# Kernel optimization log

Measured on AMD Instinct MI355X. Metric: run time of the kernel, lower is better.

The kernel has to match this reference:

```python
import jax, jax.numpy as jnp
import numpy as np

NUM_HEADS = 8

def rotate_half(x):
    # interleaved rotate: pairs (x0,x1)->(-x1,x0)
    x1 = x[..., ::2]
    x2 = x[..., 1::2]
    return jnp.stack((-x2, x1), axis=-1).reshape(x.shape)

def rope_cos_sin(seq_len, head_dim, dtype, base=10000.0):
    idx = jnp.arange(0, head_dim, 2, dtype=dtype)
    inv_freq = 1.0 / base ** (idx / head_dim)
    t = jnp.arange(seq_len, dtype=dtype)
    freqs = t[:, None] * inv_freq[None, :]            # (L, hd/2)
    emb = jnp.concatenate([freqs, freqs], axis=-1)    # (L, hd) -- NOTE: cat, not interleave (faithful to source)
    return jnp.cos(emb)[None, None], jnp.sin(emb)[None, None]  # (1,1,L,hd)

def setup_inputs() -> dict:
    key = jax.random.key(0)
    ks = jax.random.split(key, 5)
    B, L, C = 2, 4096, 512
    s_in = 1.0 / np.sqrt(C)
    return {
        "x": jax.random.normal(ks[0], (B, L, C), dtype=jnp.float32),
        "qkv_w": jax.random.normal(ks[1], (3 * C, C), dtype=jnp.float32) * s_in,
        "qkv_b": jnp.zeros((3 * C,), dtype=jnp.float32),
        "proj_w": jax.random.normal(ks[2], (C, C), dtype=jnp.float32) * s_in,
        "proj_b": jnp.zeros((C,), dtype=jnp.float32),
    }

def reference(x, qkv_w, qkv_b, proj_w, proj_b):
    B, L, C = x.shape
    H = NUM_HEADS
    hd = C // H
    scale = hd ** -0.5
    qkv = x @ qkv_w.T + qkv_b                          # (B,L,3C)
    qkv = qkv.reshape(B, L, 3, H, hd).transpose(2, 0, 3, 1, 4)  # (3,B,H,L,hd)
    q, k, v = qkv[0], qkv[1], qkv[2]
    cos, sin = rope_cos_sin(L, hd, x.dtype)
    q = q * cos + rotate_half(q) * sin
    k = k * cos + rotate_half(k) * sin
    attn = jnp.einsum('bhqd,bhkd->bhqk', q, k) * scale  # (B,H,L,L)
    attn = jax.nn.softmax(attn, axis=-1)
    out = jnp.einsum('bhqk,bhkd->bhqd', attn, v)        # (B,H,L,hd)
    out = out.transpose(0, 2, 1, 3).reshape(B, L, C)
    return out @ proj_w.T + proj_b
```

## Files before the change

### kernel.cpp

```cpp
#include <hip/hip_runtime.h>
#include <hip/hip_bf16.h>


typedef __attribute__((ext_vector_type(8))) short short8;
typedef __attribute__((ext_vector_type(4))) short short4v;
typedef __attribute__((ext_vector_type(4))) float floatx4;

#define MFMA(a, b, c)   __builtin_amdgcn_mfma_f32_16x16x32_bf16((a), (b), (c), 0, 0, 0)
#define MFMA16(a, b, c) __builtin_amdgcn_mfma_f32_16x16x16bf16_1k((a), (b), (c), 0, 0, 0)

__device__ __forceinline__ float fast_exp2(float x) {
#if __has_builtin(__builtin_amdgcn_exp2f)
    return __builtin_amdgcn_exp2f(x);
#else
    float r; asm("v_exp_f32 %0, %1" : "=v"(r) : "v"(x)); return r;
#endif
}

__device__ __forceinline__ unsigned short f2bf(float f) {
    unsigned int u = __builtin_bit_cast(unsigned int, f);
    return (unsigned short)((u + 0x7fffu + ((u >> 16) & 1u)) >> 16);
}
__device__ __forceinline__ unsigned int pack2(float lo, float hi) {
    __hip_bfloat162 h = __float22bfloat162_rn(make_float2(lo, hi));
    unsigned int r;
    __builtin_memcpy(&r, &h, 4);
    return r;
}

__global__ __launch_bounds__(256) void conv_pack(
    const float* __restrict__ src, ushort* __restrict__ dst, int n8)
{
    int i = blockIdx.x * blockDim.x + threadIdx.x;
    if (i >= n8) return;
    const int row = i >> 6, col0 = (i & 63) * 8;
    const float4* s = (const float4*)(src + (size_t)row * 512 + col0);
    float4 a = s[0], b = s[1];
    uint4 r = { pack2(a.x, a.y), pack2(a.z, a.w), pack2(b.x, b.y), pack2(b.z, b.w) };
    const int l = (row & 15) + 16 * ((col0 >> 3) & 3);
    const size_t off = (size_t)(row >> 4) * 8192 + (size_t)(col0 >> 5) * 512 + l * 8;
    *(uint4*)(dst + off) = r;
}

__global__ __launch_bounds__(256) void build_rope(float2* __restrict__ lut) {
    int i = blockIdx.x * 256 + threadIdx.x;
    int pos = i >> 5, j = i & 31;
    float invf = exp2f(-0.41524101186f * (float)j);
    float s, c;
    sincosf((float)pos * invf, &s, &c);
    lut[i] = make_float2(c, s);
}

__global__ __launch_bounds__(256) void qkv_rope(
    const ushort* __restrict__ xb,
    const ushort* __restrict__ wb,
    const float* __restrict__ bias,
    const float2* __restrict__ lut,
    ushort* __restrict__ q, ushort* __restrict__ k, ushort* __restrict__ vt,
    int G, int h0)
{
    __shared__ __align__(16) ushort vtile[64][136];
    const int w_id = threadIdx.x >> 6;
    const int lane = threadIdx.x & 63;
    const int lr = lane & 15, quad = lane >> 4;
    const int m0 = blockIdx.x * 128 + w_id * 32;
    const int sec = blockIdx.y / G, hl = blockIdx.y % G;
    const int wc0 = sec * 512 + (h0 + hl) * 64;

    floatx4 acc[2][4] = {};
    const ushort* xa = xb + (size_t)(m0 >> 4) * 8192 + lane * 8;
    const ushort* wbase = wb + (size_t)(wc0 >> 4) * 8192 + lane * 8;
    for (int kk = 0; kk < 16; ++kk) {
        short8 a0 = *(const short8*)(xa + kk * 512);
        short8 a1 = *(const short8*)(xa + 8192 + kk * 512);
#pragma unroll
        for (int nt = 0; nt < 4; ++nt) {
            short8 b = *(const short8*)(wbase + (size_t)nt * 8192 + kk * 512);
            acc[0][nt] = MFMA(a0, b, acc[0][nt]);
            acc[1][nt] = MFMA(a1, b, acc[1][nt]);
        }
    }

    if (sec < 2) {
#pragma unroll
        for (int mt = 0; mt < 2; ++mt)
#pragma unroll
            for (int nt = 0; nt < 4; ++nt) {
                const int d = nt * 16 + lr;
                const float bv = bias[wc0 + d];
#pragma unroll
                for (int r = 0; r < 4; ++r) {
                    const int row = m0 + mt * 16 + quad * 4 + r;
                    const int b_ = row >> 12;
                    const int pos = row & 4095;
                    float val = acc[mt][nt][r] + bv;
                    const size_t bhl = (size_t)(b_ * G + hl);
                    float partner = __shfl_xor(val, 1);
                    float2 cs = lut[(pos << 5) | (d & 31)];
                    float rh = (d & 1) ? partner : -partner;
                    float rv = val * cs.x + rh * cs.y;
                    if (sec == 0) {
                        rv *= 0.18033688011112042f;
                        q[(bhl * 4096 + pos) * 64 + d] = f2bf(rv);
                    } else {
                        const int idx = (pos >> 5) * 2048 + ((pos >> 4) & 1) * 1024
                                      + (d >> 5) * 512 + ((d >> 3) & 3) * 128
                                      + (pos & 15) * 8 + (d & 7);
                        k[bhl * 262144 + idx] = f2bf(rv);
                    }
                }
            }
    } else {
#pragma unroll
        for (int mt = 0; mt < 2; ++mt)
#pragma unroll
            for (int nt = 0; nt < 4; ++nt) {
                const int d = nt * 16 + lr;
                const float bv = bias[wc0 + d];
                short4v v4;
#pragma unroll
                for (int r = 0; r < 4; ++r)
                    v4[r] = (short)f2bf(acc[mt][nt][r] + bv);
                *(short4v*)&vtile[d][w_id * 32 + mt * 16 + quad * 4] = v4;
            }
        __syncthreads();
        const int m0b = blockIdx.x * 128;
        const int bb = m0b >> 12;
        const int pos0 = m0b & 4095;
        const size_t bhl = (size_t)(bb * G + hl);
        const int dt = w_id;
        ushort* vb = vt + bhl * 262144 + dt * 512 + lane * 8;
#pragma unroll
        for (int j = 0; j < 4; ++j) {
            const int col = j * 32 + quad * 4;
            short4v a = *(const short4v*)&vtile[dt * 16 + lr][col];
            short4v b = *(const short4v*)&vtile[dt * 16 + lr][col + 16];
            short8 vv = __builtin_shufflevector(a, b, 0, 1, 2, 3, 4, 5, 6, 7);
            *(short8*)(vb + ((pos0 >> 5) + j) * 2048) = vv;
        }
    }
}

__global__ __launch_bounds__(256, 3) void flash_attn(
    const ushort* __restrict__ q, const ushort* __restrict__ k,
    const ushort* __restrict__ vt, ushort* __restrict__ o,
    int G, int h0)
{
    __shared__ __align__(16) float mb[65][33];
    const int kh = threadIdx.x >> 6;
    const int lane = threadIdx.x & 63;
    const int lr = lane & 15, quad = lane >> 4;
    const int nbh = 2 * G;
    const int bhl = blockIdx.x % nbh;
    const int qtile = blockIdx.x / nbh;
    const int b_ = bhl / G, hl = bhl % G;
    const int q0 = qtile * 32;

    const ushort* qp = q + (size_t)bhl * 262144;
    const int hcol = (h0 + hl) * 64;
    ushort* opp = o + (size_t)(((b_ << 12) + q0) >> 4) * 8192 + (hcol >> 5) * 512;
    const ushort* kpw = k + (size_t)bhl * 262144 + kh * 65536 + lane * 8;
    const ushort* vpw = vt + (size_t)bhl * 262144 + kh * 65536 + lane * 8;

    short8 qf[2][2];
#pragma unroll
    for (int nn = 0; nn < 2; ++nn) {
        const ushort* qb = qp + (size_t)(q0 + 16 * nn + lr) * 64 + quad * 8;
        qf[nn][0] = *(const short8*)qb;
        qf[nn][1] = *(const short8*)(qb + 32);
    }

    floatx4 oacc[4][2] = {};
    float lsum[2] = {0.f, 0.f};
    short8 ka0[2][2], ka1[2][2];
    short8 va[4];

    auto ldK = [&](int c, short8 (&ka)[2][2]) {
        const ushort* kb = kpw + c * 2048;
        ka[0][0] = *(const short8*)(kb);
        ka[0][1] = *(const short8*)(kb + 512);
        ka[1][0] = *(const short8*)(kb + 1024);
        ka[1][1] = *(const short8*)(kb + 1536);
    };
    auto ldV = [&](int c) {
        const ushort* vb = vpw + c * 2048;
#pragma unroll
        for (int dt = 0; dt < 4; ++dt)
            va[dt] = *(const short8*)(vb + dt * 512);
    };
    auto process = [&](short8 (&ka)[2][2]) {
#pragma unroll
        for (int t = 0; t < 2; ++t) {
#pragma unroll
            for (int nn = 0; nn < 2; ++nn) {
                floatx4 s = {};
                s = MFMA(ka[t][0], qf[nn][0], s);
                s = MFMA(ka[t][1], qf[nn][1], s);
                float p0 = fast_exp2(s[0]), p1 = fast_exp2(s[1]);
                float p2 = fast_exp2(s[2]), p3 = fast_exp2(s[3]);
                lsum[nn] += (p0 + p1) + (p2 + p3);
                uint2 u = { pack2(p0, p1), pack2(p2, p3) };
                short4v pf = __builtin_bit_cast(short4v, u);
#pragma unroll
                for (int dt = 0; dt < 4; ++dt) {
                    short4v vf = (t == 0)
                        ? __builtin_shufflevector(va[dt], va[dt], 0, 1, 2, 3)
                        : __builtin_shufflevector(va[dt], va[dt], 4, 5, 6, 7);
                    oacc[dt][nn] = MFMA16(vf, pf, oacc[dt][nn]);
                }
            }
        }
    };

    ldK(0, ka0);
    for (int it = 0; it < 30; it += 2) {
        ldV(it);
        ldK(it + 1, ka1);
        process(ka0);
        ldV(it + 1);
        ldK(it + 2, ka0);
        process(ka1);
    }
    ldV(30); ldK(31, ka1); process(ka0);
    ldV(31); process(ka1);

    lsum[0] += __shfl_xor(lsum[0], 16); lsum[0] += __shfl_xor(lsum[0], 32);
    lsum[1] += __shfl_xor(lsum[1], 16); lsum[1] += __shfl_xor(lsum[1], 32);

    __syncthreads();
    if (kh == 3) {
#pragma unroll
        for (int dt = 0; dt < 4; ++dt)
#pragma unroll
            for (int nn = 0; nn < 2; ++nn)
#pragma unroll
                for (int r = 0; r < 4; ++r)
                    mb[16 * dt + 4 * quad + r][16 * nn + lr] = oacc[dt][nn][r];
        if (quad == 0) {
            mb[64][lr] = lsum[0];
            mb[64][16 + lr] = lsum[1];
        }
    }
    __syncthreads();
    if (kh == 2) {
#pragma unroll
        for (int dt = 0; dt < 4; ++dt)
#pragma unroll
            for (int nn = 0; nn < 2; ++nn)
#pragma unroll
                for (int r = 0; r < 4; ++r)
                    mb[16 * dt + 4 * quad + r][16 * nn + lr] += oacc[dt][nn][r];
        if (quad == 0) {
            mb[64][lr] += lsum[0];
            mb[64][16 + lr] += lsum[1];
        }
    }
    __syncthreads();
    if (kh == 1) {
#pragma unroll
        for (int dt = 0; dt < 4; ++dt)
#pragma unroll
            for (int nn = 0; nn < 2; ++nn)
#pragma unroll
                for (int r = 0; r < 4; ++r)
                    mb[16 * dt + 4 * quad + r][16 * nn + lr] += oacc[dt][nn][r];
        if (quad == 0) {
            mb[64][lr] += lsum[0];
            mb[64][16 + lr] += lsum[1];
        }
    }
    __syncthreads();
    if (kh == 0) {
        float inv0 = 1.0f / (lsum[0] + mb[64][lr]);
        float inv1 = 1.0f / (lsum[1] + mb[64][16 + lr]);
#pragma unroll
        for (int dt = 0; dt < 4; ++dt)
#pragma unroll
            for (int nn = 0; nn < 2; ++nn) {
                float inv = nn ? inv1 : inv0;
                float v0 = (oacc[dt][nn][0] + mb[16 * dt + 4 * quad + 0][16 * nn + lr]) * inv;
                float v1 = (oacc[dt][nn][1] + mb[16 * dt + 4 * quad + 1][16 * nn + lr]) * inv;
                float v2 = (oacc[dt][nn][2] + mb[16 * dt + 4 * quad + 2][16 * nn + lr]) * inv;
                float v3 = (oacc[dt][nn][3] + mb[16 * dt + 4 * quad + 3][16 * nn + lr]) * inv;
                uint2 u = { pack2(v0, v1), pack2(v2, v3) };
                const int cg = 16 * dt + 4 * quad;
                *(uint2*)(opp + (size_t)nn * 8192 + (cg >> 5) * 512
                          + (lr + 16 * ((cg >> 3) & 3)) * 8 + (cg & 7)) = u;
            }
    }
}

__global__ __launch_bounds__(256) void proj_gemm(
    const ushort* __restrict__ o,
    const ushort* __restrict__ wb,
    const float* __restrict__ bias,
    float* __restrict__ out)
{
    const int w_id = threadIdx.x >> 6;
    const int lane = threadIdx.x & 63;
    const int lr = lane & 15, quad = lane >> 4;
    const int m0 = blockIdx.x * 128 + w_id * 32;
    const int n0 = blockIdx.y * 64;

    floatx4 acc[2][4] = {};
    const ushort* oa = o + (size_t)(m0 >> 4) * 8192 + lane * 8;
    const ushort* wbase = wb + (size_t)(n0 >> 4) * 8192 + lane * 8;
    for (int kk = 0; kk < 16; ++kk) {
        short8 a0 = *(const short8*)(oa + kk * 512);
        short8 a1 = *(const short8*)(oa + 8192 + kk * 512);
#pragma unroll
        for (int nt = 0; nt < 4; ++nt) {
            short8 b = *(const short8*)(wbase + (size_t)nt * 8192 + kk * 512);
            acc[0][nt] = MFMA(a0, b, acc[0][nt]);
            acc[1][nt] = MFMA(a1, b, acc[1][nt]);
        }
    }
#pragma unroll
    for (int mt = 0; mt < 2; ++mt)
#pragma unroll
        for (int nt = 0; nt < 4; ++nt) {
            const int n = n0 + nt * 16 + lr;
            const float bv = bias[n];
#pragma unroll
            for (int r = 0; r < 4; ++r)
                out[(size_t)(m0 + mt * 16 + quad * 4 + r) * 512 + n] = acc[mt][nt][r] + bv;
        }
}

extern "C" void kernel_launch(void* const* d_in, const int* in_sizes, int n_in,
                              void* d_out, int out_size, void* d_ws, size_t ws_size,
                              hipStream_t stream)
{
    const float* x      = (const float*)d_in[0];
    const float* qkv_w  = (const float*)d_in[1];
    const float* qkv_b  = (const float*)d_in[2];
    const float* proj_w = (const float*)d_in[3];
    const float* proj_b = (const float*)d_in[4];
    float* out = (float*)d_out;

    const size_t MB = (size_t)1 << 20;
    ushort* base = (ushort*)d_ws;
    int G;
    ushort *xb, *o, *wb, *pwb, *q, *k, *vt;
    if (ws_size >= 34 * MB) {
        G = 8;
        xb = base; o = base;
        wb  = base + 4194304;
        pwb = wb + 786432;
        q   = pwb + 262144;
        k   = q + (size_t)G * 524288;
        vt  = k + (size_t)G * 524288;
    } else {
        G = (ws_size >= 30 * MB) ? 4 : (ws_size >= 24 * MB) ? 2 : 1;
        xb  = base;
        o   = base + 4194304;
        wb  = o + 4194304;
        pwb = wb + 786432;
        q   = pwb + 262144;
        k   = q + (size_t)G * 524288;
        vt  = k + (size_t)G * 524288;
    }

    float2* lut = (float2*)d_out;
    build_rope<<<512, 256, 0, stream>>>(lut);

    conv_pack<<<2048, 256, 0, stream>>>(x, xb, 524288);
    conv_pack<<<384, 256, 0, stream>>>(qkv_w, wb, 98304);
    conv_pack<<<128, 256, 0, stream>>>(proj_w, pwb, 32768);

    for (int h0 = 0; h0 < 8; h0 += G) {
        qkv_rope<<<dim3(64, 3 * G), 256, 0, stream>>>(xb, wb, qkv_b, lut, q, k, vt, G, h0);
        flash_attn<<<128 * 2 * G, 256, 0, stream>>>(q, k, vt, o, G, h0);
    }
    proj_gemm<<<dim3(64, 8), 256, 0, stream>>>(o, pwb, proj_b, out);
}
```

Measured before the change: 219.9 us.

## Switch flash attention to 32x32x16 MFMA with matching K/V layouts

Replaces the 16x16 MFMA tiling in the attention kernel with 32x32x16 bf16 MFMAs. A single 32x32 score tile now covers all 32 queries, and the PV product accumulates into two 16-float accumulators. The K and V^T global layouts written by the QKV kernel are re-swizzled so each lane's 8-element loads feed the 32x32 operand layout directly, and the epilogue reduction and output store are remapped to match. This is meant to cut MFMA issue count and per-instruction overhead, at the cost of larger accumulators and a different register and exp scheduling pattern.

```diff
diff --git a/kernel.cpp b/kernel.cpp
--- a/kernel.cpp
+++ b/kernel.cpp
@@ -2,12 +2,13 @@
 #include <hip/hip_bf16.h>
 
 
-typedef __attribute__((ext_vector_type(8))) short short8;
-typedef __attribute__((ext_vector_type(4))) short short4v;
-typedef __attribute__((ext_vector_type(4))) float floatx4;
+typedef __attribute__((ext_vector_type(8)))  short short8;
+typedef __attribute__((ext_vector_type(4)))  short short4v;
+typedef __attribute__((ext_vector_type(4)))  float floatx4;
+typedef __attribute__((ext_vector_type(16))) float floatx16;
 
 #define MFMA(a, b, c)   __builtin_amdgcn_mfma_f32_16x16x32_bf16((a), (b), (c), 0, 0, 0)
-#define MFMA16(a, b, c) __builtin_amdgcn_mfma_f32_16x16x16bf16_1k((a), (b), (c), 0, 0, 0)
+#define MFMA32(a, b, c) __builtin_amdgcn_mfma_f32_32x32x16_bf16((a), (b), (c), 0, 0, 0)
 
 __device__ __forceinline__ float fast_exp2(float x) {
 #if __has_builtin(__builtin_amdgcn_exp2f)
@@ -103,9 +104,9 @@
                         rv *= 0.18033688011112042f;
                         q[(bhl * 4096 + pos) * 64 + d] = f2bf(rv);
                     } else {
-                        const int idx = (pos >> 5) * 2048 + ((pos >> 4) & 1) * 1024
-                                      + (d >> 5) * 512 + ((d >> 3) & 3) * 128
-                                      + (pos & 15) * 8 + (d & 7);
+                        const int idx = (pos >> 5) * 2048 + (d >> 4) * 512
+                                      + ((pos & 31) + 32 * ((d >> 3) & 1)) * 8
+                                      + (d & 7);
                         k[bhl * 262144 + idx] = f2bf(rv);
                     }
                 }
@@ -126,17 +127,22 @@
         __syncthreads();
         const int m0b = blockIdx.x * 128;
         const int bb = m0b >> 12;
-        const int pos0 = m0b & 4095;
+        const int c0g = (m0b & 4095) >> 5;
         const size_t bhl = (size_t)(bb * G + hl);
-        const int dt = w_id;
-        ushort* vb = vt + bhl * 262144 + dt * 512 + lane * 8;
-#pragma unroll
-        for (int j = 0; j < 4; ++j) {
-            const int col = j * 32 + quad * 4;
-            short4v a = *(const short4v*)&vtile[dt * 16 + lr][col];
-            short4v b = *(const short4v*)&vtile[dt * 16 + lr][col + 16];
+        const int gid = threadIdx.x >> 6;
+        const int l = threadIdx.x & 63;
+        const int h = l >> 5;
+        ushort* vb = vt + bhl * 262144 + l * 8;
+#pragma unroll
+        for (int i = 0; i < 4; ++i) {
+            const int combo = i * 4 + gid;
+            const int c4 = combo >> 2, dt = (combo >> 1) & 1, s = combo & 1;
+            const int d = dt * 32 + (l & 31);
+            const int colbase = c4 * 32 + s * 16 + 4 * h;
+            short4v a = *(const short4v*)&vtile[d][colbase];
+            short4v b = *(const short4v*)&vtile[d][colbase + 8];
             short8 vv = __builtin_shufflevector(a, b, 0, 1, 2, 3, 4, 5, 6, 7);
-            *(short8*)(vb + ((pos0 >> 5) + j) * 2048) = vv;
+            *(short8*)(vb + (size_t)(c0g + c4) * 2048 + dt * 1024 + s * 512) = vv;
         }
     }
 }
@@ -149,7 +155,7 @@
     __shared__ __align__(16) float mb[65][33];
     const int kh = threadIdx.x >> 6;
     const int lane = threadIdx.x & 63;
-    const int lr = lane & 15, quad = lane >> 4;
+    const int ln31 = lane & 31, h = lane >> 5;
     const int nbh = 2 * G;
     const int bhl = blockIdx.x % nbh;
     const int qtile = blockIdx.x / nbh;
@@ -162,54 +168,58 @@
     const ushort* kpw = k + (size_t)bhl * 262144 + kh * 65536 + lane * 8;
     const ushort* vpw = vt + (size_t)bhl * 262144 + kh * 65536 + lane * 8;
 
-    short8 qf[2][2];
-#pragma unroll
-    for (int nn = 0; nn < 2; ++nn) {
-        const ushort* qb = qp + (size_t)(q0 + 16 * nn + lr) * 64 + quad * 8;
-        qf[nn][0] = *(const short8*)qb;
-        qf[nn][1] = *(const short8*)(qb + 32);
-    }
-
-    floatx4 oacc[4][2] = {};
-    float lsum[2] = {0.f, 0.f};
-    short8 ka0[2][2], ka1[2][2];
+    short8 qf[4];
+    {
+        const ushort* qb = qp + (size_t)(q0 + ln31) * 64 + h * 8;
+        qf[0] = *(const short8*)(qb);
+        qf[1] = *(const short8*)(qb + 16);
+        qf[2] = *(const short8*)(qb + 32);
+        qf[3] = *(const short8*)(qb + 48);
+    }
+
+    floatx16 oacc[2] = {};
+    float lsum = 0.f;
+    short8 ka0[4], ka1[4];
     short8 va[4];
 
-    auto ldK = [&](int c, short8 (&ka)[2][2]) {
+    auto ldK = [&](int c, short8 (&ka)[4]) {
         const ushort* kb = kpw + c * 2048;
-        ka[0][0] = *(const short8*)(kb);
-        ka[0][1] = *(const short8*)(kb + 512);
-        ka[1][0] = *(const short8*)(kb + 1024);
-        ka[1][1] = *(const short8*)(kb + 1536);
+        ka[0] = *(const short8*)(kb);
+        ka[1] = *(const short8*)(kb + 512);
+        ka[2] = *(const short8*)(kb + 1024);
+        ka[3] = *(const short8*)(kb + 1536);
     };
     auto ldV = [&](int c) {
         const ushort* vb = vpw + c * 2048;
-#pragma unroll
-        for (int dt = 0; dt < 4; ++dt)
-            va[dt] = *(const short8*)(vb + dt * 512);
+        va[0] = *(const short8*)(vb);
+        va[1] = *(const short8*)(vb + 512);
+        va[2] = *(const short8*)(vb + 1024);
+        va[3] = *(const short8*)(vb + 1536);
     };
-    auto process = [&](short8 (&ka)[2][2]) {
-#pragma unroll
-        for (int t = 0; t < 2; ++t) {
-#pragma unroll
-            for (int nn = 0; nn < 2; ++nn) {
-                floatx4 s = {};
-                s = MFMA(ka[t][0], qf[nn][0], s);
-                s = MFMA(ka[t][1], qf[nn][1], s);
-                float p0 = fast_exp2(s[0]), p1 = fast_exp2(s[1]);
-                float p2 = fast_exp2(s[2]), p3 = fast_exp2(s[3]);
-                lsum[nn] += (p0 + p1) + (p2 + p3);
-                uint2 u = { pack2(p0, p1), pack2(p2, p3) };
-                short4v pf = __builtin_bit_cast(short4v, u);
-#pragma unroll
-                for (int dt = 0; dt < 4; ++dt) {
-                    short4v vf = (t == 0)
-                        ? __builtin_shufflevector(va[dt], va[dt], 0, 1, 2, 3)
-                        : __builtin_shufflevector(va[dt], va[dt], 4, 5, 6, 7);
-                    oacc[dt][nn] = MFMA16(vf, pf, oacc[dt][nn]);
-                }
-            }
-        }
+    auto process = [&](short8 (&ka)[4]) {
+        floatx16 s = {};
+        s = MFMA32(ka[0], qf[0], s);
+        s = MFMA32(ka[1], qf[1], s);
+        s = MFMA32(ka[2], qf[2], s);
+        s = MFMA32(ka[3], qf[3], s);
+        float p[16];
+#pragma unroll
+        for (int r = 0; r < 16; ++r) p[r] = fast_exp2(s[r]);
+        float t0 = (p[0] + p[1]) + (p[2] + p[3]);
+        float t1 = (p[4] + p[5]) + (p[6] + p[7]);
+        float t2 = (p[8] + p[9]) + (p[10] + p[11]);
+        float t3 = (p[12] + p[13]) + (p[14] + p[15]);
+        lsum += (t0 + t1) + (t2 + t3);
+        uint4 u0 = { pack2(p[0], p[1]), pack2(p[2], p[3]),
+                     pack2(p[4], p[5]), pack2(p[6], p[7]) };
+        uint4 u1 = { pack2(p[8], p[9]), pack2(p[10], p[11]),
+                     pack2(p[12], p[13]), pack2(p[14], p[15]) };
+        short8 pb0 = __builtin_bit_cast(short8, u0);
+        short8 pb1 = __builtin_bit_cast(short8, u1);
+        oacc[0] = MFMA32(va[0], pb0, oacc[0]);
+        oacc[0] = MFMA32(va[1], pb1, oacc[0]);
+        oacc[1] = MFMA32(va[2], pb0, oacc[1]);
+        oacc[1] = MFMA32(va[3], pb1, oacc[1]);
     };
 
     ldK(0, ka0);
@@ -224,68 +234,50 @@
     ldV(30); ldK(31, ka1); process(ka0);
     ldV(31); process(ka1);
 
-    lsum[0] += __shfl_xor(lsum[0], 16); lsum[0] += __shfl_xor(lsum[0], 32);
-    lsum[1] += __shfl_xor(lsum[1], 16); lsum[1] += __shfl_xor(lsum[1], 32);
+    lsum += __shfl_xor(lsum, 32);
 
     __syncthreads();
     if (kh == 3) {
 #pragma unroll
-        for (int dt = 0; dt < 4; ++dt)
-#pragma unroll
-            for (int nn = 0; nn < 2; ++nn)
-#pragma unroll
-                for (int r = 0; r < 4; ++r)
-                    mb[16 * dt + 4 * quad + r][16 * nn + lr] = oacc[dt][nn][r];
-        if (quad == 0) {
-            mb[64][lr] = lsum[0];
-            mb[64][16 + lr] = lsum[1];
-        }
+        for (int dt = 0; dt < 2; ++dt)
+#pragma unroll
+            for (int r = 0; r < 16; ++r)
+                mb[dt * 32 + (r & 3) + 8 * (r >> 2) + 4 * h][ln31] = oacc[dt][r];
+        if (h == 0) mb[64][ln31] = lsum;
     }
     __syncthreads();
     if (kh == 2) {
 #pragma unroll
-        for (int dt = 0; dt < 4; ++dt)
-#pragma unroll
-            for (int nn = 0; nn < 2; ++nn)
-#pragma unroll
-                for (int r = 0; r < 4; ++r)
-                    mb[16 * dt + 4 * quad + r][16 * nn + lr] += oacc[dt][nn][r];
-        if (quad == 0) {
-            mb[64][lr] += lsum[0];
-            mb[64][16 + lr] += lsum[1];
-        }
+        for (int dt = 0; dt < 2; ++dt)
+#pragma unroll
+            for (int r = 0; r < 16; ++r)
+                mb[dt * 32 + (r & 3) + 8 * (r >> 2) + 4 * h][ln31] += oacc[dt][r];
+        if (h == 0) mb[64][ln31] += lsum;
     }
     __syncthreads();
     if (kh == 1) {
 #pragma unroll
-        for (int dt = 0; dt < 4; ++dt)
-#pragma unroll
-            for (int nn = 0; nn < 2; ++nn)
-#pragma unroll
-                for (int r = 0; r < 4; ++r)
-                    mb[16 * dt + 4 * quad + r][16 * nn + lr] += oacc[dt][nn][r];
-        if (quad == 0) {
-            mb[64][lr] += lsum[0];
-            mb[64][16 + lr] += lsum[1];
-        }
+        for (int dt = 0; dt < 2; ++dt)
+#pragma unroll
+            for (int r = 0; r < 16; ++r)
+                mb[dt * 32 + (r & 3) + 8 * (r >> 2) + 4 * h][ln31] += oacc[dt][r];
+        if (h == 0) mb[64][ln31] += lsum;
     }
     __syncthreads();
     if (kh == 0) {
-        float inv0 = 1.0f / (lsum[0] + mb[64][lr]);
-        float inv1 = 1.0f / (lsum[1] + mb[64][16 + lr]);
-#pragma unroll
-        for (int dt = 0; dt < 4; ++dt)
-#pragma unroll
-            for (int nn = 0; nn < 2; ++nn) {
-                float inv = nn ? inv1 : inv0;
-                float v0 = (oacc[dt][nn][0] + mb[16 * dt + 4 * quad + 0][16 * nn + lr]) * inv;
-                float v1 = (oacc[dt][nn][1] + mb[16 * dt + 4 * quad + 1][16 * nn + lr]) * inv;
-                float v2 = (oacc[dt][nn][2] + mb[16 * dt + 4 * quad + 2][16 * nn + lr]) * inv;
-                float v3 = (oacc[dt][nn][3] + mb[16 * dt + 4 * quad + 3][16 * nn + lr]) * inv;
+        const float inv = 1.0f / (lsum + mb[64][ln31]);
+#pragma unroll
+        for (int dt = 0; dt < 2; ++dt)
+#pragma unroll
+            for (int g = 0; g < 4; ++g) {
+                const int d0 = dt * 32 + 8 * g + 4 * h;
+                float v0 = (oacc[dt][4 * g + 0] + mb[d0 + 0][ln31]) * inv;
+                float v1 = (oacc[dt][4 * g + 1] + mb[d0 + 1][ln31]) * inv;
+                float v2 = (oacc[dt][4 * g + 2] + mb[d0 + 2][ln31]) * inv;
+                float v3 = (oacc[dt][4 * g + 3] + mb[d0 + 3][ln31]) * inv;
                 uint2 u = { pack2(v0, v1), pack2(v2, v3) };
-                const int cg = 16 * dt + 4 * quad;
-                *(uint2*)(opp + (size_t)nn * 8192 + (cg >> 5) * 512
-                          + (lr + 16 * ((cg >> 3) & 3)) * 8 + (cg & 7)) = u;
+                *(uint2*)(opp + (size_t)(ln31 >> 4) * 8192 + dt * 512
+                          + ((ln31 & 15) + 16 * g) * 8 + 4 * h) = u;
             }
     }
 }
```

Measured after the change: 222.4 us. Within noise of the previous version (+1.1%).
